# Kernel optimization log

Measured on AMD Instinct MI355X. Metric: run time of the kernel, lower is better.

## Reference

```python
import jax, jax.numpy as jnp
import numpy as np

FEAT_STRIDE = 32  # 520 // 16
POOL = 7          # adaptive_avg_pool2d target (7,7)
C = 8             # channels consumed as (2 classes x 4 coords)


def setup_inputs() -> dict:
    key = jax.random.key(0)
    k1, k2, k3 = jax.random.split(key, 3)
    H = W = 1024
    conv_out = jax.random.normal(k1, (1, C, H, W), dtype=jnp.float32)
    n = 8192
    # sample pixel-space coords in [0, H*FEAT_STRIDE) and sort so min<=max per axis
    ys = jnp.sort(jax.random.randint(k2, (n, 2), 0, H * FEAT_STRIDE), axis=1)
    xs = jnp.sort(jax.random.randint(k3, (n, 2), 0, W * FEAT_STRIDE), axis=1)
    rois = jnp.stack([ys[:, 0], xs[:, 0], ys[:, 1], xs[:, 1]], axis=1).astype(jnp.int64)
    return {"conv_out": conv_out, "rois": rois}


def _adaptive_bounds(start, length):
    # PyTorch adaptive_avg_pool2d bin edges over [start, start+length)
    j = jnp.arange(POOL)
    lo = start + (j * length) // POOL
    hi = start + ((j + 1) * length + POOL - 1) // POOL  # ceil div
    return lo, hi


def _forward(conv_out, rois):
    r = rois // FEAT_STRIDE
    x = conv_out[0]  # [C, H, W]
    # summed-area table, padded so sat[:, y, x] = sum over [0:y, 0:x)
    sat = jnp.pad(jnp.cumsum(jnp.cumsum(x, axis=1), axis=2),
                  ((0, 0), (1, 0), (1, 0)))  # [C, H+1, W+1]

    def pool_one(roi):
        ymin, xmin = roi[0], roi[1]
        ymax, xmax = roi[2] + 1, roi[3] + 1  # exclusive ends
        ylo, yhi = _adaptive_bounds(ymin, ymax - ymin)
        xlo, xhi = _adaptive_bounds(xmin, xmax - xmin)
        # 7x7 bin sums via inclusion-exclusion on SAT -> [C,7,7]
        s = (sat[:, yhi[:, None], xhi[None, :]]
             - sat[:, ylo[:, None], xhi[None, :]]
             - sat[:, yhi[:, None], xlo[None, :]]
             + sat[:, ylo[:, None], xlo[None, :]])
        area = ((yhi - ylo)[:, None] * (xhi - xlo)[None, :]).astype(s.dtype)
        block7 = s / area                       # adaptive_avg_pool2d -> (7,7)
        return block7.mean(axis=(1, 2))         # adaptive_avg_pool2d -> (1,1), [C]

    pooled = jax.vmap(pool_one)(r)              # [n, C]
    return pooled.reshape(-1, 2, 4)


def reference(conv_out, rois):
    return _forward(conv_out, rois)
```

## Files before the change

### kernel.cpp

```cpp
#include <hip/hip_runtime.h>
#include <cstddef>
#include <cstdint>

#define SATW_PAD 1026
#define W8   8200
#define W8P  8208
#define NCH  8
#define STRIP 16
#define NSTRIP (W8P / STRIP)

__global__ __launch_bounds__(256) void rowscan_kernel(const float* __restrict__ in,
                                                      float* __restrict__ sat) {
    const int y    = blockIdx.x;
    const int t    = threadIdx.x;
    const int lane = t & 63;
    const int wv   = t >> 6;

    __shared__ float lds[NCH][1024];

    for (int k = 0; k < 2; ++k) {
        const int c = wv * 2 + k;
        const float4* r4 = (const float4*)(in + ((size_t)c * 1024 + y) * 1024);
        double chunkbase = 0.0;
#pragma unroll
        for (int j = 0; j < 4; ++j) {
            float4 a = r4[lane + 64 * j];
            double v0 = a.x, v1 = a.y, v2 = a.z, v3 = a.w;
            double s = v0 + v1 + v2 + v3;
            double ps = s;
#pragma unroll
            for (int off = 1; off < 64; off <<= 1) {
                double n = __shfl_up(ps, off, 64);
                if (lane >= off) ps += n;
            }
            double base = chunkbase + ps - s;
            double p0 = base + v0, p1 = p0 + v1, p2 = p1 + v2, p3 = p2 + v3;
            ((float4*)lds[c])[lane + 64 * j] =
                make_float4((float)p0, (float)p1, (float)p2, (float)p3);
            chunkbase += __shfl(ps, 63, 64);
        }
    }
    __syncthreads();

    float* orow = sat + (size_t)(y + 1) * W8P;
    for (int f4 = t; f4 < W8P / 4; f4 += 256) {
        int f = f4 * 4;
        float4 o;
        float* po = (float*)&o;
#pragma unroll
        for (int j = 0; j < 4; ++j) {
            int ff = f + j;
            int x = ff >> 3, c = ff & 7;
            po[j] = (x >= 1 && x <= 1024) ? lds[c][x - 1] : 0.0f;
        }
        ((float4*)orow)[f4] = o;
    }
}

__global__ __launch_bounds__(256) void colscan_block(float* __restrict__ sat) {
    const int t    = threadIdx.x;
    const int lane = t & 63;
    const int w    = t >> 6;
    const int rg   = lane >> 2;
    const int q    = lane & 3;
    const int c0   = blockIdx.x * STRIP + q * 4;

    float* p0 = sat + (size_t)(1 + w * 256 + rg * 16) * W8P + c0;

    float4 v[16];
#pragma unroll
    for (int k = 0; k < 16; ++k)
        v[k] = *(const float4*)(p0 + (size_t)k * W8P);

    double T0 = 0, T1 = 0, T2 = 0, T3 = 0;
#pragma unroll
    for (int k = 0; k < 16; ++k) {
        T0 += v[k].x; T1 += v[k].y; T2 += v[k].z; T3 += v[k].w;
    }

    double i0 = T0, i1 = T1, i2 = T2, i3 = T3;
#pragma unroll
    for (int s = 4; s <= 32; s <<= 1) {
        double a0 = __shfl_up(i0, s, 64), a1 = __shfl_up(i1, s, 64);
        double a2 = __shfl_up(i2, s, 64), a3 = __shfl_up(i3, s, 64);
        if (lane >= s) { i0 += a0; i1 += a1; i2 += a2; i3 += a3; }
    }
    double e0 = i0 - T0, e1 = i1 - T1, e2 = i2 - T2, e3 = i3 - T3;

    __shared__ double wt[4][4][4];
    if (lane >= 60) {
        wt[w][q][0] = i0; wt[w][q][1] = i1; wt[w][q][2] = i2; wt[w][q][3] = i3;
    }
    __syncthreads();
    double b0 = e0, b1 = e1, b2 = e2, b3 = e3;
    for (int w2 = 0; w2 < w; ++w2) {
        b0 += wt[w2][q][0]; b1 += wt[w2][q][1];
        b2 += wt[w2][q][2]; b3 += wt[w2][q][3];
    }

#pragma unroll
    for (int k = 0; k < 16; ++k) {
        b0 += v[k].x; b1 += v[k].y; b2 += v[k].z; b3 += v[k].w;
        *(float4*)(p0 + (size_t)k * W8P) =
            make_float4((float)b0, (float)b1, (float)b2, (float)b3);
    }

    if (t < 4) {
        int cz = blockIdx.x * STRIP + t * 4;
        *(float4*)(sat + cz) = make_float4(0.f, 0.f, 0.f, 0.f);
    }
}

__global__ __launch_bounds__(256) void pool_kernel(const float* __restrict__ sat,
                                                   const int* __restrict__ rois,
                                                   float* __restrict__ out,
                                                   int n_roi) {
    int lane = threadIdx.x & 63;
    int roi  = (blockIdx.x * blockDim.x + threadIdx.x) >> 6;
    if (roi >= n_roi) return;

    const int4 rv = ((const int4*)rois)[roi];
    int ymin = rv.x >> 5;
    int xmin = rv.y >> 5;
    int Ly   = (rv.z >> 5) + 1 - ymin;
    int Lx   = (rv.w >> 5) + 1 - xmin;

    float acc[NCH];
#pragma unroll
    for (int c = 0; c < NCH; ++c) acc[c] = 0.0f;

    if (lane < 49) {
        int by = lane / 7;
        int bx = lane - by * 7;
        int ylo = ymin + (by * Ly) / 7;
        int yhi = ymin + ((by + 1) * Ly + 6) / 7;
        int xlo = xmin + (bx * Lx) / 7;
        int xhi = xmin + ((bx + 1) * Lx + 6) / 7;
        float inv = 1.0f / (float)((yhi - ylo) * (xhi - xlo));

        float4 a[2], b[2], c4[2], d[2];
        const float4* hh = (const float4*)(sat + ((size_t)yhi * SATW_PAD + xhi) * NCH);
        const float4* lh = (const float4*)(sat + ((size_t)ylo * SATW_PAD + xhi) * NCH);
        const float4* hl = (const float4*)(sat + ((size_t)yhi * SATW_PAD + xlo) * NCH);
        const float4* ll = (const float4*)(sat + ((size_t)ylo * SATW_PAD + xlo) * NCH);
        a[0] = hh[0]; a[1] = hh[1];
        b[0] = lh[0]; b[1] = lh[1];
        c4[0] = hl[0]; c4[1] = hl[1];
        d[0] = ll[0]; d[1] = ll[1];
        const float* fa = (const float*)a;
        const float* fb = (const float*)b;
        const float* fc = (const float*)c4;
        const float* fd = (const float*)d;
#pragma unroll
        for (int c = 0; c < NCH; ++c)
            acc[c] = (fa[c] - fb[c] - fc[c] + fd[c]) * inv;
    }

#pragma unroll
    for (int off = 32; off; off >>= 1) {
#pragma unroll
        for (int c = 0; c < NCH; ++c) acc[c] += __shfl_down(acc[c], off, 64);
    }

    if (lane == 0) {
        const float k = 1.0f / 49.0f;
        float4* po = (float4*)(out + (size_t)roi * NCH);
        po[0] = make_float4(acc[0] * k, acc[1] * k, acc[2] * k, acc[3] * k);
        po[1] = make_float4(acc[4] * k, acc[5] * k, acc[6] * k, acc[7] * k);
    }
}

extern "C" void kernel_launch(void* const* d_in, const int* in_sizes, int n_in,
                              void* d_out, int out_size, void* d_ws, size_t ws_size,
                              hipStream_t stream) {
    const float* conv = (const float*)d_in[0];
    const int*   rois = (const int*)d_in[1];
    float*       out  = (float*)d_out;
    int n_roi = in_sizes[1] / 4;

    float* sat = (float*)d_ws;

    rowscan_kernel<<<1024, 256, 0, stream>>>(conv, sat);
    colscan_block<<<NSTRIP, 256, 0, stream>>>(sat);
    pool_kernel<<<(n_roi + 3) / 4, 256, 0, stream>>>(sat, rois, out, n_roi);
}
```

Before: 114.0 us.

## Bucket ROIs by ymin row so pool kernel gathers SAT rows with locality

Builds a histogram of ROI ymin rows inside rowscan block 0, then runs a single-block counting sort that produces a permutation of ROI indices. The pool kernel processes ROIs in that order, so neighbouring waves read nearby SAT rows and the cache hit rate on the random gathers should rise. In exchange it adds a serial one-block kernel launch, atomics and an extra indirection per ROI, and rowscan block 0 takes longer.

Measured after the change: 128.8 us. 13.0% more time.

```diff
diff --git a/kernel.cpp b/kernel.cpp
--- a/kernel.cpp
+++ b/kernel.cpp
@@ -9,8 +9,15 @@
 #define STRIP 16
 #define NSTRIP (W8P / STRIP)
 
+#define SAT_BYTES ((size_t)1025 * W8P * 4)
+#define HIST_OFF  ((SAT_BYTES + 255) & ~(size_t)255)
+#define ORDER_OFF (HIST_OFF + 4096)
+
 __global__ __launch_bounds__(256) void rowscan_kernel(const float* __restrict__ in,
-                                                      float* __restrict__ sat) {
+                                                      float* __restrict__ sat,
+                                                      const int* __restrict__ rois,
+                                                      int* __restrict__ hist,
+                                                      int n_roi) {
     const int y    = blockIdx.x;
     const int t    = threadIdx.x;
     const int lane = t & 63;
@@ -55,6 +62,48 @@
         }
         ((float4*)orow)[f4] = o;
     }
+
+    if (y == 0) {
+        __shared__ int h[1024];
+        for (int i = t; i < 1024; i += 256) h[i] = 0;
+        __syncthreads();
+        for (int i = t; i < n_roi; i += 256) {
+            int ym = ((const int4*)rois)[i].x >> 5;
+            atomicAdd(&h[ym], 1);
+        }
+        __syncthreads();
+        for (int i = t; i < 1024; i += 256) hist[i] = h[i];
+    }
+}
+
+__global__ __launch_bounds__(1024) void sortscatter_kernel(const int* __restrict__ hist,
+                                                           const int* __restrict__ rois,
+                                                           int* __restrict__ order,
+                                                           int n_roi) {
+    const int t = threadIdx.x;
+    const int lane = t & 63, w = t >> 6;
+    __shared__ int off[1024];
+    __shared__ int wsum[16];
+
+    int v = hist[t];
+    int ps = v;
+#pragma unroll
+    for (int s = 1; s < 64; s <<= 1) {
+        int n = __shfl_up(ps, s, 64);
+        if (lane >= s) ps += n;
+    }
+    if (lane == 63) wsum[w] = ps;
+    __syncthreads();
+    int base = 0;
+    for (int i = 0; i < w; ++i) base += wsum[i];
+    off[t] = base + ps - v;
+    __syncthreads();
+
+    for (int i = t; i < n_roi; i += 1024) {
+        int key = ((const int4*)rois)[i].x >> 5;
+        int pos = atomicAdd(&off[key], 1);
+        order[pos] = i;
+    }
 }
 
 __global__ __launch_bounds__(256) void colscan_block(float* __restrict__ sat) {
@@ -113,11 +162,13 @@
 
 __global__ __launch_bounds__(256) void pool_kernel(const float* __restrict__ sat,
                                                    const int* __restrict__ rois,
+                                                   const int* __restrict__ order,
                                                    float* __restrict__ out,
                                                    int n_roi) {
     int lane = threadIdx.x & 63;
-    int roi  = (blockIdx.x * blockDim.x + threadIdx.x) >> 6;
-    if (roi >= n_roi) return;
+    int wid  = (blockIdx.x * blockDim.x + threadIdx.x) >> 6;
+    if (wid >= n_roi) return;
+    int roi = order[wid];
 
     const int4 rv = ((const int4*)rois)[roi];
     int ymin = rv.x >> 5;
@@ -178,9 +229,12 @@
     float*       out  = (float*)d_out;
     int n_roi = in_sizes[1] / 4;
 
-    float* sat = (float*)d_ws;
-
-    rowscan_kernel<<<1024, 256, 0, stream>>>(conv, sat);
+    float* sat   = (float*)d_ws;
+    int*   hist  = (int*)((char*)d_ws + HIST_OFF);
+    int*   order = (int*)((char*)d_ws + ORDER_OFF);
+
+    rowscan_kernel<<<1024, 256, 0, stream>>>(conv, sat, rois, hist, n_roi);
+    sortscatter_kernel<<<1, 1024, 0, stream>>>(hist, rois, order, n_roi);
     colscan_block<<<NSTRIP, 256, 0, stream>>>(sat);
-    pool_kernel<<<(n_roi + 3) / 4, 256, 0, stream>>>(sat, rois, out, n_roi);
-}
+    pool_kernel<<<(n_roi + 3) / 4, 256, 0, stream>>>(sat, rois, order, out, n_roi);
+}
```
